# Performance work log

Hardware: AMD Instinct MI355X
Metric: run time of the kernel (lower is better)

Reference implementation:

```python
import jax, jax.numpy as jnp
import numpy as np

DIM = 512
HEADS = 8
DIM_HEAD = 64
INNER = HEADS * DIM_HEAD
CHUNK = 32
EPS = 1e-5


def _peg_conv(x, w, b):
    # x: (B, N, C); depthwise conv1d k=3 pad=1 applied on chunks of 32
    B, N, C = x.shape
    ns = -(-N // CHUNK)
    xp = jnp.pad(x, ((0, 0), (0, ns * CHUNK - N), (0, 0)))
    xp = xp.reshape(B * ns, CHUNK, C).transpose(0, 2, 1)  # (B*ns, C, 32)
    y = jax.lax.conv_general_dilated(
        xp, w, window_strides=(1,), padding=((1, 1),),
        dimension_numbers=("NCH", "OIH", "NCH"), feature_group_count=C)
    y = y + b[None, :, None]
    y = y.transpose(0, 2, 1).reshape(B, ns * CHUNK, C)[:, :N, :]
    return y


def _peg1d(x, w, b):
    p1 = _peg_conv(x, w, b)
    sx = jnp.roll(x, CHUNK // 2, axis=1)
    p2 = jnp.roll(_peg_conv(sx, w, b), -(CHUNK // 2), axis=1)
    return x + p1 + p2


def setup_inputs() -> dict:
    key = jax.random.key(0)
    ks = jax.random.split(key, 8)
    B, N, M = 2, 4096, 1024
    x = jax.random.normal(ks[0], (B, N, DIM), dtype=jnp.float32)
    mem = jax.random.normal(ks[1], (B, M, DIM), dtype=jnp.float32)
    w_qkv = jax.random.normal(ks[2], (DIM, 3 * INNER), dtype=jnp.float32) * 0.02
    w_out = jax.random.normal(ks[3], (INNER, DIM), dtype=jnp.float32) * 0.02
    b_out = jnp.zeros((DIM,), dtype=jnp.float32)
    ln_g = jnp.ones((DIM,), dtype=jnp.float32)
    ln_b = jnp.zeros((DIM,), dtype=jnp.float32)
    pk_w = jax.random.normal(ks[4], (DIM, 1, 3), dtype=jnp.float32) * 0.1
    pk_b = jnp.zeros((DIM,), dtype=jnp.float32)
    pv_w = jax.random.normal(ks[5], (DIM, 1, 3), dtype=jnp.float32) * 0.1
    pv_b = jnp.zeros((DIM,), dtype=jnp.float32)
    return {"x": x, "mem": mem, "ln_g": ln_g, "ln_b": ln_b,
            "w_qkv": w_qkv, "w_out": w_out, "b_out": b_out,
            "pk_w": pk_w, "pk_b": pk_b, "pv_w": pv_w, "pv_b": pv_b}


def reference(x, mem, ln_g, ln_b, w_qkv, w_out, b_out, pk_w, pk_b, pv_w, pv_b):
    B, N, _ = x.shape
    # LayerNorm
    mu = jnp.mean(x, axis=-1, keepdims=True)
    var = jnp.mean(jnp.square(x - mu), axis=-1, keepdims=True)
    xn = (x - mu) * jax.lax.rsqrt(var + EPS) * ln_g + ln_b
    qkv = xn @ w_qkv  # (B, N, 3*INNER)
    q, k, v = jnp.split(qkv, 3, axis=-1)
    # memory concat
    k = jnp.concatenate((k, mem), axis=1)
    v = jnp.concatenate((v, mem), axis=1)
    # PEG1D positional conv on k,v (excluding cls token at position 0)
    k = jnp.concatenate((k[:, :1, :], _peg1d(k[:, 1:, :], pk_w, pk_b)), axis=1)
    v = jnp.concatenate((v[:, :1, :], _peg1d(v[:, 1:, :], pv_w, pv_b)), axis=1)
    # split heads: b n (h d) -> b h n d
    Nk = k.shape[1]
    qh = q.reshape(B, N, HEADS, DIM_HEAD).transpose(0, 2, 1, 3)
    kh = k.reshape(B, Nk, HEADS, DIM_HEAD).transpose(0, 2, 1, 3)
    vh = v.reshape(B, Nk, HEADS, DIM_HEAD).transpose(0, 2, 1, 3)
    scale = DIM_HEAD ** -0.5
    dots = jnp.einsum("bhnd,bhmd->bhnm", qh, kh) * scale
    attn = jax.nn.softmax(dots, axis=-1)
    out = jnp.einsum("bhnm,bhmd->bhnd", attn, vh)
    out = out.transpose(0, 2, 1, 3).reshape(B, N, INNER)
    return out @ w_out + b_out
```

## Files before the change

### kernel.cpp

```cpp
#include <hip/hip_runtime.h>
#include <hip/hip_bf16.h>

typedef short short8 __attribute__((ext_vector_type(8)));
typedef __bf16 bf16x8 __attribute__((ext_vector_type(8)));
typedef float f32x4 __attribute__((ext_vector_type(4)));
typedef float f32x8 __attribute__((ext_vector_type(8)));
typedef float f32x16 __attribute__((ext_vector_type(16)));
typedef unsigned int uint4v __attribute__((ext_vector_type(4)));

#define SEQ_N 4096
#define NKEYS 5120
#define PEG_L 5119
#define NSPLIT 2
#define KEYS_PER_SPLIT 2560
#define NT_SPLIT 40

__device__ __forceinline__ float b2f(unsigned short s){
  union{unsigned u; float f;} v; v.u = ((unsigned)s)<<16; return v.f;
}
__device__ __forceinline__ unsigned short f2b(float f){
  unsigned u = __builtin_bit_cast(unsigned, f);
  u += 0x7fffu + ((u>>16)&1u);
  return (unsigned short)(u>>16);
}
__device__ __forceinline__ unsigned cvtpk(float lo, float hi){
  unsigned r;
  asm("v_cvt_pk_bf16_f32 %0, %1, %2" : "=v"(r) : "v"(lo), "v"(hi));
  return r;
}

__global__ void k_transpose_w(const float* __restrict__ src, unsigned short* __restrict__ dst,
                              int K, int Ncols){
  __shared__ float t[32][33];
  int tx = threadIdx.x, ty = threadIdx.y;
  int bx = blockIdx.x, by = blockIdx.y;
  #pragma unroll
  for (int i=0;i<4;i++){
    int r = by*32 + ty + 8*i, c = bx*32 + tx;
    t[ty+8*i][tx] = src[(size_t)r*Ncols + c];
  }
  __syncthreads();
  #pragma unroll
  for (int i=0;i<4;i++){
    int r = bx*32 + ty + 8*i, c = by*32 + tx;
    dst[(size_t)r*K + c] = f2b(t[tx][ty+8*i]);
  }
}

__global__ __launch_bounds__(256) void k_layernorm(const float* __restrict__ x,
    const float* __restrict__ g, const float* __restrict__ bb,
    unsigned short* __restrict__ xn){
  int w = threadIdx.x >> 6, l = threadIdx.x & 63;
  int row = blockIdx.x*4 + w;
  const float* xr = x + (size_t)row*512 + l*8;
  f32x4 a = *(const f32x4*)xr;
  f32x4 c4 = *(const f32x4*)(xr+4);
  float s = a[0]+a[1]+a[2]+a[3]+c4[0]+c4[1]+c4[2]+c4[3];
  #pragma unroll
  for (int d=1; d<64; d<<=1) s += __shfl_xor(s, d);
  float mu = s * (1.0f/512.0f);
  float vs = 0.f;
  #pragma unroll
  for (int i=0;i<4;i++){ float d0=a[i]-mu; vs += d0*d0; }
  #pragma unroll
  for (int i=0;i<4;i++){ float d0=c4[i]-mu; vs += d0*d0; }
  #pragma unroll
  for (int d=1; d<64; d<<=1) vs += __shfl_xor(vs, d);
  float rstd = rsqrtf(vs*(1.0f/512.0f) + 1e-5f);
  const float* gp = g + l*8;
  const float* bp = bb + l*8;
  unsigned short o[8];
  #pragma unroll
  for (int i=0;i<8;i++){
    float xi = (i<4)? a[i] : c4[i-4];
    o[i] = f2b((xi-mu)*rstd*gp[i] + bp[i]);
  }
  *(short8*)(xn + (size_t)row*512 + l*8) = *(short8*)o;
}

__global__ void k_memcat(const float* __restrict__ mem,
                         unsigned short* __restrict__ kf, unsigned short* __restrict__ vf){
  size_t e0 = ((size_t)blockIdx.x*256 + threadIdx.x)*8;
  f32x4 a = *(const f32x4*)(mem+e0);
  f32x4 c4 = *(const f32x4*)(mem+e0+4);
  unsigned short o[8];
  #pragma unroll
  for (int i=0;i<8;i++) o[i] = f2b((i<4)? a[i] : c4[i-4]);
  int c = (int)(e0 & 511);
  size_t row = e0 >> 9;
  size_t b = row >> 10, r = row & 1023;
  size_t dst = ((b*NKEYS) + 4096 + r)*512 + c;
  *(short8*)(kf+dst) = *(short8*)o;
  *(short8*)(vf+dst) = *(short8*)o;
}

template<int EPI>
__global__ __launch_bounds__(256) void k_gemm2(const unsigned short* __restrict__ A,
    const unsigned short* __restrict__ BT, const float* __restrict__ bias,
    unsigned short* __restrict__ qb, unsigned short* __restrict__ kf,
    unsigned short* __restrict__ vf, float* __restrict__ outf){
  __shared__ unsigned short Al[128][72];
  __shared__ unsigned short Bl[128][72];
  const int tid = threadIdx.x;
  const int w = tid>>6, l = tid&63, m = l&15, hh = l>>4;
  const int m0 = blockIdx.x*128, n0 = blockIdx.y*128;
  f32x4 acc[2][8];
  #pragma unroll
  for (int mt=0; mt<2; ++mt)
    #pragma unroll
    for (int nt=0; nt<8; ++nt) acc[mt][nt] = f32x4{0.f,0.f,0.f,0.f};

  for (int kt=0; kt<8; ++kt){
    short8 av[4], bv[4];
    #pragma unroll
    for (int i=0;i<4;++i){
      int c = tid + i*256;
      int row = c >> 3, c8 = (c & 7)*8;
      av[i] = *(const short8*)(A  + (size_t)(m0+row)*512 + kt*64 + c8);
      bv[i] = *(const short8*)(BT + (size_t)(n0+row)*512 + kt*64 + c8);
    }
    __syncthreads();
    #pragma unroll
    for (int i=0;i<4;++i){
      int c = tid + i*256;
      int row = c >> 3, c8 = (c & 7)*8;
      *(short8*)&Al[row][c8] = av[i];
      *(short8*)&Bl[row][c8] = bv[i];
    }
    __syncthreads();
    #pragma unroll
    for (int ks=0; ks<2; ++ks){
      bf16x8 af[2];
      #pragma unroll
      for (int mt=0; mt<2; ++mt)
        af[mt] = *(const bf16x8*)&Al[w*32 + mt*16 + m][ks*32 + hh*8];
      #pragma unroll
      for (int nt=0; nt<8; ++nt){
        bf16x8 bfv = *(const bf16x8*)&Bl[nt*16+m][ks*32 + hh*8];
        #pragma unroll
        for (int mt=0; mt<2; ++mt)
          acc[mt][nt] = __builtin_amdgcn_mfma_f32_16x16x32_bf16(af[mt], bfv, acc[mt][nt], 0,0,0);
      }
    }
  }
  #pragma unroll
  for (int mt=0; mt<2; ++mt){
    #pragma unroll
    for (int nt=0; nt<8; ++nt){
      #pragma unroll
      for (int j=0; j<4; ++j){
        int grow = m0 + w*32 + mt*16 + 4*hh + j;
        int gcol = n0 + nt*16 + m;
        float v = acc[mt][nt][j];
        if (EPI==0){
          int b = grow >> 12, n = grow & 4095;
          if (gcol < 512)       qb[(size_t)grow*512 + gcol] = f2b(v);
          else if (gcol < 1024) kf[((size_t)b*NKEYS + n)*512 + (gcol-512)]  = f2b(v);
          else                  vf[((size_t)b*NKEYS + n)*512 + (gcol-1024)] = f2b(v);
        } else {
          outf[(size_t)grow*512 + gcol] = v + bias[gcol];
        }
      }
    }
  }
}

__global__ __launch_bounds__(256) void k_peg(const unsigned short* __restrict__ in,
    const float* __restrict__ w3, const float* __restrict__ bias,
    unsigned short* __restrict__ out){
  int idx = blockIdx.x*256 + threadIdx.x;
  int cg = idx & 63;
  int i  = (idx >> 6) % NKEYS;
  int b  = (idx >> 6) / NKEYS;
  int c0 = cg*8;
  const unsigned short* base = in + (size_t)b*NKEYS*512 + c0;
  unsigned short* op = out + ((size_t)b*NKEYS + i)*512 + c0;
  if (i == 0){ *(short8*)op = *(const short8*)base; return; }
  int j = i - 1;
  float wv0[8], wv1[8], wv2[8], bv[8], acc[8];
  #pragma unroll
  for (int k2=0;k2<8;k2++){
    wv0[k2] = w3[(c0+k2)*3 + 0];
    wv1[k2] = w3[(c0+k2)*3 + 1];
    wv2[k2] = w3[(c0+k2)*3 + 2];
    bv[k2]  = bias[c0+k2];
  }
  short8 xc = *(const short8*)(base + (size_t)i*512);
  #pragma unroll
  for (int k2=0;k2<8;k2++)
    acc[k2] = b2f((unsigned short)xc[k2]) * (1.0f + 2.0f*wv1[k2]) + 2.0f*bv[k2];
  int r = j & 31;
  int jj = j + 16; if (jj >= PEG_L) jj -= PEG_L;
  int r2 = jj & 31;
  if (r > 0){
    short8 xl = *(const short8*)(base + (size_t)j*512);
    #pragma unroll
    for (int k2=0;k2<8;k2++) acc[k2] += wv0[k2]*b2f((unsigned short)xl[k2]);
  }
  if (r < 31 && j+1 < PEG_L){
    short8 xr = *(const short8*)(base + (size_t)(j+2)*512);
    #pragma unroll
    for (int k2=0;k2<8;k2++) acc[k2] += wv2[k2]*b2f((unsigned short)xr[k2]);
  }
  if (r2 > 0){
    int p = jj - 17; if (p < 0) p += PEG_L;
    short8 xl = *(const short8*)(base + (size_t)(p+1)*512);
    #pragma unroll
    for (int k2=0;k2<8;k2++) acc[k2] += wv0[k2]*b2f((unsigned short)xl[k2]);
  }
  if (r2 < 31 && jj+1 < PEG_L){
    int p = jj - 15; if (p < 0) p += PEG_L;
    short8 xr = *(const short8*)(base + (size_t)(p+1)*512);
    #pragma unroll
    for (int k2=0;k2<8;k2++) acc[k2] += wv2[k2]*b2f((unsigned short)xr[k2]);
  }
  unsigned short o[8];
  #pragma unroll
  for (int k2=0;k2<8;k2++) o[k2] = f2b(acc[k2]);
  *(short8*)op = *(short8*)o;
}

__global__ __launch_bounds__(256) void k_vtrans(const unsigned short* __restrict__ vp,
                                                unsigned short* __restrict__ vpT){
  __shared__ unsigned short t[64][72];
  const int bh = blockIdx.y, b = bh>>3, h = bh&7;
  const int k0 = blockIdx.x*64;
  const int tid = threadIdx.x;
  #pragma unroll
  for (int it=0; it<2; ++it){
    int idx = tid + it*256;
    int key = idx>>3, dg = idx&7;
    short8 v = *(const short8*)(vp + ((size_t)b*NKEYS + k0+key)*512 + h*64 + dg*8);
    #pragma unroll
    for (int jj=0;jj<8;++jj) t[dg*8+jj][key] = (unsigned short)v[jj];
  }
  __syncthreads();
  #pragma unroll
  for (int it=0; it<2; ++it){
    int idx = tid + it*256;
    int d = idx>>3, kg = idx&7;
    short8 v = *(const short8*)&t[d][kg*8];
    *(short8*)(vpT + ((size_t)bh*64 + d)*NKEYS + k0 + kg*8) = v;
  }
}

__global__ __launch_bounds__(256, 4) void k_attn(
    const unsigned short* __restrict__ qb,
    const unsigned short* __restrict__ kp,
    const unsigned short* __restrict__ vpT,
    unsigned short* __restrict__ oP,
    float* __restrict__ ml){
  __shared__ unsigned short Kl[2][64][72];
  __shared__ unsigned short Vl[2][64][72];
  const int tid = threadIdx.x;
  const int w = tid >> 6, lid = tid & 63;
  const int lq = lid & 31, hi = lid >> 5;
  const int bh = blockIdx.y, b = bh >> 3, h = bh & 7;
  const int sp = blockIdx.z;
  const int q = blockIdx.x*128 + w*32 + lq;

  bf16x8 qreg[4];
  {
    const unsigned short* qr = qb + (size_t)(b*SEQ_N + q)*512 + h*64 + hi*8;
    #pragma unroll
    for (int dt=0; dt<4; ++dt) qreg[dt] = *(const bf16x8*)(qr + dt*16);
  }

  f32x16 o0 = {}, o1 = {};
  f32x8 lsum8 = {};
  float mraw = -3.0e38f;

  const int srow = tid >> 2, sg = tid & 3;
  const unsigned short* kst = kp + (size_t)b*NKEYS*512 + h*64
                              + (size_t)(sp*KEYS_PER_SPLIT)*512 + (size_t)srow*512 + sg*8;
  const unsigned short* vst = vpT + (size_t)bh*64*NKEYS + (size_t)srow*NKEYS
                              + sp*KEYS_PER_SPLIT + sg*8;

  {
    short8 a0 = *(const short8*)(kst);
    short8 a1 = *(const short8*)(kst + 32);
    short8 v0 = *(const short8*)(vst);
    short8 v1 = *(const short8*)(vst + 32);
    *(short8*)&Kl[0][srow][sg*8]    = a0;
    *(short8*)&Kl[0][srow][32+sg*8] = a1;
    *(short8*)&Vl[0][srow][sg*8]    = v0;
    *(short8*)&Vl[0][srow][32+sg*8] = v1;
  }
  __syncthreads();

  const float c2 = 0.18033688011f;
  int cur = 0;
  for (int kt=0; kt<NT_SPLIT; ++kt){
    short8 a0, a1, v0s, v1s;
    const bool pf = (kt+1) < NT_SPLIT;
    if (pf){
      const unsigned short* kn = kst + (size_t)(kt+1)*64*512;
      const unsigned short* vn = vst + (size_t)(kt+1)*64;
      a0  = *(const short8*)(kn);
      a1  = *(const short8*)(kn + 32);
      v0s = *(const short8*)(vn);
      v1s = *(const short8*)(vn + 32);
    }

    f32x16 s0 = {}, s1 = {};
    #pragma unroll
    for (int dt=0; dt<4; ++dt){
      bf16x8 kf0 = *(const bf16x8*)&Kl[cur][lq][dt*16 + hi*8];
      s0 = __builtin_amdgcn_mfma_f32_32x32x16_bf16(kf0, qreg[dt], s0, 0,0,0);
    }
    #pragma unroll
    for (int dt=0; dt<4; ++dt){
      bf16x8 kf1 = *(const bf16x8*)&Kl[cur][32+lq][dt*16 + hi*8];
      s1 = __builtin_amdgcn_mfma_f32_32x32x16_bf16(kf1, qreg[dt], s1, 0,0,0);
    }

    f32x8 sa0 = __builtin_shufflevector(s0, s0, 0,1,2,3,4,5,6,7);
    f32x8 sb0 = __builtin_shufflevector(s0, s0, 8,9,10,11,12,13,14,15);
    f32x8 sa1 = __builtin_shufflevector(s1, s1, 0,1,2,3,4,5,6,7);
    f32x8 sb1 = __builtin_shufflevector(s1, s1, 8,9,10,11,12,13,14,15);
    f32x8 mx8 = __builtin_elementwise_max(__builtin_elementwise_max(sa0, sb0),
                                          __builtin_elementwise_max(sa1, sb1));
    float pm = fmaxf(fmaxf(fmaxf(mx8[0],mx8[1]), fmaxf(mx8[2],mx8[3])),
                     fmaxf(fmaxf(mx8[4],mx8[5]), fmaxf(mx8[6],mx8[7])));

    if (!__all(pm <= mraw + 64.0f)){
      float pg = fmaxf(pm, __shfl_xor(pm, 32, 64));
      float mnew = fmaxf(mraw, pg);
      float al = __builtin_amdgcn_exp2f((mraw - mnew)*c2);
      #pragma unroll
      for (int i=0;i<16;++i){ o0[i]*=al; o1[i]*=al; }
      #pragma unroll
      for (int i=0;i<8;++i) lsum8[i] *= al;
      mraw = mnew;
    }
    const float nmc = -(mraw * c2);
    #pragma unroll
    for (int i=0;i<16;++i){
      s0[i] = __builtin_amdgcn_exp2f(fmaf(s0[i], c2, nmc));
      s1[i] = __builtin_amdgcn_exp2f(fmaf(s1[i], c2, nmc));
    }
    {
      f32x8 pa0 = __builtin_shufflevector(s0, s0, 0,1,2,3,4,5,6,7);
      f32x8 pb0 = __builtin_shufflevector(s0, s0, 8,9,10,11,12,13,14,15);
      f32x8 pa1 = __builtin_shufflevector(s1, s1, 0,1,2,3,4,5,6,7);
      f32x8 pb1 = __builtin_shufflevector(s1, s1, 8,9,10,11,12,13,14,15);
      lsum8 += (pa0 + pb0) + (pa1 + pb1);
    }

    #pragma unroll
    for (int sl=0; sl<4; ++sl){
      const f32x16& sv = (sl < 2) ? s0 : s1;
      const int rb = (sl & 1)*8;
      unsigned w0 = cvtpk(sv[rb+0], sv[rb+1]);
      unsigned w1 = cvtpk(sv[rb+2], sv[rb+3]);
      unsigned w2 = cvtpk(sv[rb+4], sv[rb+5]);
      unsigned w3 = cvtpk(sv[rb+6], sv[rb+7]);
      unsigned u0 = hi ? w0 : w2;
      unsigned u1 = hi ? w1 : w3;
      unsigned su0 = __shfl_xor(u0, 32, 64);
      unsigned su1 = __shfl_xor(u1, 32, 64);
      unsigned e0 = hi ? su0 : w0;
      unsigned e1 = hi ? su1 : w1;
      unsigned e2 = hi ? w2 : su0;
      unsigned e3 = hi ? w3 : su1;
      uint4v wv = {e0, e1, e2, e3};
      bf16x8 pb = __builtin_bit_cast(bf16x8, wv);
      bf16x8 vf0 = *(const bf16x8*)&Vl[cur][lq][sl*16 + hi*8];
      o0 = __builtin_amdgcn_mfma_f32_32x32x16_bf16(vf0, pb, o0, 0,0,0);
      bf16x8 vf1 = *(const bf16x8*)&Vl[cur][32+lq][sl*16 + hi*8];
      o1 = __builtin_amdgcn_mfma_f32_32x32x16_bf16(vf1, pb, o1, 0,0,0);
    }

    if (pf){
      *(short8*)&Kl[cur^1][srow][sg*8]    = a0;
      *(short8*)&Kl[cur^1][srow][32+sg*8] = a1;
      *(short8*)&Vl[cur^1][srow][sg*8]    = v0s;
      *(short8*)&Vl[cur^1][srow][32+sg*8] = v1s;
    }
    __syncthreads();
    cur ^= 1;
  }

  f32x4 l4 = f32x4{lsum8[0],lsum8[1],lsum8[2],lsum8[3]} + f32x4{lsum8[4],lsum8[5],lsum8[6],lsum8[7]};
  float lsum = (l4[0]+l4[1]) + (l4[2]+l4[3]);
  const float lt = lsum + __shfl_xor(lsum, 32, 64);
  const float inv = __builtin_amdgcn_rcpf(lt);
  unsigned short* op = oP + (((size_t)(sp*16 + bh)*SEQ_N + q)*64);
  #pragma unroll
  for (int r=0; r<16; r+=2){
    const int dloc = (r&3) + 8*(r>>2) + 4*hi;
    *(unsigned*)(op + dloc)      = cvtpk(o0[r]*inv, o0[r+1]*inv);
    *(unsigned*)(op + 32 + dloc) = cvtpk(o1[r]*inv, o1[r+1]*inv);
  }
  float* mlp = ml + ((size_t)(sp*16 + bh)*SEQ_N + q)*2;
  mlp[0] = mraw;
  mlp[1] = lt;
}

__global__ __launch_bounds__(256) void k_combine(const unsigned short* __restrict__ oP,
    const float* __restrict__ ml, unsigned short* __restrict__ attnb){
  const float c2 = 0.18033688011f;
  int idx = blockIdx.x*256 + threadIdx.x;
  int dg = idx & 7;
  int qbh = idx >> 3;
  int q = qbh & 4095;
  int bh = qbh >> 12;
  int b = bh >> 3, h = bh & 7;
  size_t i0 = ((size_t)bh*SEQ_N + q);
  size_t i1 = ((size_t)(16 + bh)*SEQ_N + q);
  short8 a = *(const short8*)(oP + i0*64 + dg*8);
  short8 c = *(const short8*)(oP + i1*64 + dg*8);
  float m0 = ml[i0*2], l0 = ml[i0*2+1];
  float m1 = ml[i1*2], l1 = ml[i1*2+1];
  float ms = fmaxf(m0, m1);
  float w0 = l0 * __builtin_amdgcn_exp2f((m0 - ms)*c2);
  float w1 = l1 * __builtin_amdgcn_exp2f((m1 - ms)*c2);
  float inv = 1.0f / (w0 + w1);
  float a0 = w0*inv, a1 = w1*inv;
  unsigned short o[8];
  #pragma unroll
  for (int k2=0;k2<8;k2++)
    o[k2] = f2b(a0*b2f((unsigned short)a[k2]) + a1*b2f((unsigned short)c[k2]));
  *(short8*)(attnb + ((size_t)(b*SEQ_N + q)*512) + h*64 + dg*8) = *(short8*)o;
}

extern "C" void kernel_launch(void* const* d_in, const int* in_sizes, int n_in,
                              void* d_out, int out_size, void* d_ws, size_t ws_size,
                              hipStream_t stream){
  const float* x     = (const float*)d_in[0];
  const float* mem   = (const float*)d_in[1];
  const float* ln_g  = (const float*)d_in[2];
  const float* ln_b  = (const float*)d_in[3];
  const float* w_qkv = (const float*)d_in[4];
  const float* w_out = (const float*)d_in[5];
  const float* b_out = (const float*)d_in[6];
  const float* pk_w  = (const float*)d_in[7];
  const float* pk_b  = (const float*)d_in[8];
  const float* pv_w  = (const float*)d_in[9];
  const float* pv_b  = (const float*)d_in[10];
  float* outp = (float*)d_out;

  char* ws = (char*)d_ws;
  size_t off = 0;
  auto alloc = [&](size_t bytes)->void*{
    void* p = ws + off; off += (bytes + 255) & ~(size_t)255; return p;
  };
  unsigned short* wqkvT = (unsigned short*)alloc((size_t)1536*512*2);
  unsigned short* woutT = (unsigned short*)alloc((size_t)512*512*2);
  unsigned short* xn    = (unsigned short*)alloc((size_t)8192*512*2);
  unsigned short* q_b   = (unsigned short*)alloc((size_t)8192*512*2);
  unsigned short* kf    = (unsigned short*)alloc((size_t)2*NKEYS*512*2);
  unsigned short* vf    = (unsigned short*)alloc((size_t)2*NKEYS*512*2);
  unsigned short* kpg   = (unsigned short*)alloc((size_t)2*NKEYS*512*2);
  unsigned short* vpg   = (unsigned short*)alloc((size_t)2*NKEYS*512*2);
  unsigned short* vpT   = (unsigned short*)alloc((size_t)2*NKEYS*512*2);
  unsigned short* attnb = (unsigned short*)alloc((size_t)8192*512*2);

  unsigned short* oP = kf;
  float* ml = (float*)((char*)kf + (size_t)NSPLIT*16*SEQ_N*64*2);

  k_transpose_w<<<dim3(48,16), dim3(32,8), 0, stream>>>(w_qkv, wqkvT, 512, 1536);
  k_transpose_w<<<dim3(16,16), dim3(32,8), 0, stream>>>(w_out, woutT, 512, 512);
  k_layernorm<<<2048, 256, 0, stream>>>(x, ln_g, ln_b, xn);
  k_memcat<<<512, 256, 0, stream>>>(mem, kf, vf);
  k_gemm2<0><<<dim3(64,12), 256, 0, stream>>>(xn, wqkvT, nullptr, q_b, kf, vf, nullptr);
  k_peg<<<2560, 256, 0, stream>>>(kf, pk_w, pk_b, kpg);
  k_peg<<<2560, 256, 0, stream>>>(vf, pv_w, pv_b, vpg);
  k_vtrans<<<dim3(80,16), 256, 0, stream>>>(vpg, vpT);
  k_attn<<<dim3(32,16,NSPLIT), 256, 0, stream>>>(q_b, kpg, vpT, oP, ml);
  k_combine<<<2048, 256, 0, stream>>>(oP, ml, attnb);
  k_gemm2<1><<<dim3(64,4), 256, 0, stream>>>(attnb, woutT, b_out, nullptr, nullptr, nullptr, outp);
}
```

Baseline: 282.3 us.

## Fuse split-attention combine into output GEMM, merge k/v PEG launches

Replaces the combine kernel with a small kernel that only computes per-row split weights, and folds the weighted merge of the two partial attention outputs into the A-tile load of the output projection GEMM. This removes the write and re-read of the combined bf16 attention buffer. The k and v PEG convolutions now run in a single launch using blockIdx.y, and the attention kernel's launch-bounds occupancy hint is lowered from 4 to 3. The trade-off is that each of the 4 output-GEMM column blocks recomputes the merge and reads both partial buffers, which adds redundant loads.

New measurement: 282.7 us. About the same (+0.1%).

```diff
diff --git a/kernel.cpp b/kernel.cpp
--- a/kernel.cpp
+++ b/kernel.cpp
@@ -98,7 +98,8 @@
 __global__ __launch_bounds__(256) void k_gemm2(const unsigned short* __restrict__ A,
     const unsigned short* __restrict__ BT, const float* __restrict__ bias,
     unsigned short* __restrict__ qb, unsigned short* __restrict__ kf,
-    unsigned short* __restrict__ vf, float* __restrict__ outf){
+    unsigned short* __restrict__ vf, float* __restrict__ outf,
+    const unsigned short* __restrict__ oPp, const float* __restrict__ comb){
   __shared__ unsigned short Al[128][72];
   __shared__ unsigned short Bl[128][72];
   const int tid = threadIdx.x;
@@ -116,7 +117,22 @@
     for (int i=0;i<4;++i){
       int c = tid + i*256;
       int row = c >> 3, c8 = (c & 7)*8;
-      av[i] = *(const short8*)(A  + (size_t)(m0+row)*512 + kt*64 + c8);
+      if (EPI==0){
+        av[i] = *(const short8*)(A + (size_t)(m0+row)*512 + kt*64 + c8);
+      } else {
+        int gr = m0 + row;
+        int b2 = gr >> 12, q = gr & 4095;
+        size_t ibase = ((size_t)(b2*8 + kt)*SEQ_N + q)*64 + c8;
+        short8 x0 = *(const short8*)(oPp + ibase);
+        short8 x1 = *(const short8*)(oPp + (size_t)16*SEQ_N*64 + ibase);
+        size_t ci = ((size_t)(b2*8 + kt)*SEQ_N + q)*2;
+        float a0 = comb[ci], a1 = comb[ci+1];
+        unsigned short t8[8];
+        #pragma unroll
+        for (int j=0;j<8;++j)
+          t8[j] = f2b(a0*b2f((unsigned short)x0[j]) + a1*b2f((unsigned short)x1[j]));
+        av[i] = *(short8*)t8;
+      }
       bv[i] = *(const short8*)(BT + (size_t)(n0+row)*512 + kt*64 + c8);
     }
     __syncthreads();
@@ -165,9 +181,16 @@
   }
 }
 
-__global__ __launch_bounds__(256) void k_peg(const unsigned short* __restrict__ in,
-    const float* __restrict__ w3, const float* __restrict__ bias,
-    unsigned short* __restrict__ out){
+__global__ __launch_bounds__(256) void k_peg(const unsigned short* __restrict__ ink,
+    const unsigned short* __restrict__ inv,
+    const float* __restrict__ w3k, const float* __restrict__ w3v,
+    const float* __restrict__ bk, const float* __restrict__ bvp,
+    unsigned short* __restrict__ outk, unsigned short* __restrict__ outv){
+  const int kv = blockIdx.y;
+  const unsigned short* in = kv ? inv : ink;
+  const float* w3 = kv ? w3v : w3k;
+  const float* bias = kv ? bvp : bk;
+  unsigned short* out = kv ? outv : outk;
   int idx = blockIdx.x*256 + threadIdx.x;
   int cg = idx & 63;
   int i  = (idx >> 6) % NKEYS;
@@ -244,7 +267,7 @@
   }
 }
 
-__global__ __launch_bounds__(256, 4) void k_attn(
+__global__ __launch_bounds__(256, 3) void k_attn(
     const unsigned short* __restrict__ qb,
     const unsigned short* __restrict__ kp,
     const unsigned short* __restrict__ vpT,
@@ -397,31 +420,20 @@
   mlp[1] = lt;
 }
 
-__global__ __launch_bounds__(256) void k_combine(const unsigned short* __restrict__ oP,
-    const float* __restrict__ ml, unsigned short* __restrict__ attnb){
+__global__ __launch_bounds__(256) void k_mlw(const float* __restrict__ ml,
+                                             float* __restrict__ comb){
   const float c2 = 0.18033688011f;
   int idx = blockIdx.x*256 + threadIdx.x;
-  int dg = idx & 7;
-  int qbh = idx >> 3;
-  int q = qbh & 4095;
-  int bh = qbh >> 12;
-  int b = bh >> 3, h = bh & 7;
-  size_t i0 = ((size_t)bh*SEQ_N + q);
-  size_t i1 = ((size_t)(16 + bh)*SEQ_N + q);
-  short8 a = *(const short8*)(oP + i0*64 + dg*8);
-  short8 c = *(const short8*)(oP + i1*64 + dg*8);
+  size_t i0 = idx;
+  size_t i1 = (size_t)16*SEQ_N + idx;
   float m0 = ml[i0*2], l0 = ml[i0*2+1];
   float m1 = ml[i1*2], l1 = ml[i1*2+1];
   float ms = fmaxf(m0, m1);
   float w0 = l0 * __builtin_amdgcn_exp2f((m0 - ms)*c2);
   float w1 = l1 * __builtin_amdgcn_exp2f((m1 - ms)*c2);
   float inv = 1.0f / (w0 + w1);
-  float a0 = w0*inv, a1 = w1*inv;
-  unsigned short o[8];
-  #pragma unroll
-  for (int k2=0;k2<8;k2++)
-    o[k2] = f2b(a0*b2f((unsigned short)a[k2]) + a1*b2f((unsigned short)c[k2]));
-  *(short8*)(attnb + ((size_t)(b*SEQ_N + q)*512) + h*64 + dg*8) = *(short8*)o;
+  comb[(size_t)idx*2]   = w0*inv;
+  comb[(size_t)idx*2+1] = w1*inv;
 }
 
 extern "C" void kernel_launch(void* const* d_in, const int* in_sizes, int n_in,
@@ -458,16 +470,16 @@
 
   unsigned short* oP = kf;
   float* ml = (float*)((char*)kf + (size_t)NSPLIT*16*SEQ_N*64*2);
+  float* comb = (float*)attnb;
 
   k_transpose_w<<<dim3(48,16), dim3(32,8), 0, stream>>>(w_qkv, wqkvT, 512, 1536);
   k_transpose_w<<<dim3(16,16), dim3(32,8), 0, stream>>>(w_out, woutT, 512, 512);
   k_layernorm<<<2048, 256, 0, stream>>>(x, ln_g, ln_b, xn);
   k_memcat<<<512, 256, 0, stream>>>(mem, kf, vf);
-  k_gemm2<0><<<dim3(64,12), 256, 0, stream>>>(xn, wqkvT, nullptr, q_b, kf, vf, nullptr);
-  k_peg<<<2560, 256, 0, stream>>>(kf, pk_w, pk_b, kpg);
-  k_peg<<<2560, 256, 0, stream>>>(vf, pv_w, pv_b, vpg);
+  k_gemm2<0><<<dim3(64,12), 256, 0, stream>>>(xn, wqkvT, nullptr, q_b, kf, vf, nullptr, nullptr, nullptr);
+  k_peg<<<dim3(2560,2), 256, 0, stream>>>(kf, vf, pk_w, pv_w, pk_b, pv_b, kpg, vpg);
   k_vtrans<<<dim3(80,16), 256, 0, stream>>>(vpg, vpT);
   k_attn<<<dim3(32,16,NSPLIT), 256, 0, stream>>>(q_b, kpg, vpT, oP, ml);
-  k_combine<<<2048, 256, 0, stream>>>(oP, ml, attnb);
-  k_gemm2<1><<<dim3(64,4), 256, 0, stream>>>(attnb, woutT, b_out, nullptr, nullptr, nullptr, outp);
-}
+  k_mlw<<<256, 256, 0, stream>>>(ml, comb);
+  k_gemm2<1><<<dim3(64,4), 256, 0, stream>>>(nullptr, woutT, b_out, nullptr, nullptr, nullptr, outp, oP, comb);
+}
```
